# Performance work log

Hardware: AMD Instinct MI355X
Metric: run time of the kernel (lower is better)

The kernel has to match this reference:

```python
import jax, jax.numpy as jnp
import numpy as np

H = 128          # h_dim
F_IN = 3 * H     # leaf/edge feature dim
N = 65536        # number of center nodes
E = 1000000      # number of leaf nodes / edges


def setup_inputs() -> dict:
    key = jax.random.key(0)
    ks = jax.random.split(key, 8)
    center_node_attr = jax.random.normal(ks[0], (N, H), jnp.float32)
    leaf_node_all = jax.random.normal(ks[1], (E, F_IN), jnp.float32)
    node_idx = jax.random.randint(ks[2], (E,), 0, N, dtype=jnp.int32)
    gcnfeats = jax.random.normal(ks[3], (N, H), jnp.float32)
    # nn.Linear default init: U(-1/sqrt(fan_in), 1/sqrt(fan_in))
    s1 = 1.0 / np.sqrt(F_IN)
    s2 = 1.0 / np.sqrt(H)
    W1 = jax.random.uniform(ks[4], (F_IN, H), jnp.float32, -s1, s1)
    b1 = jax.random.uniform(ks[5], (H,), jnp.float32, -s1, s1)
    W2 = jax.random.uniform(ks[6], (H, H), jnp.float32, -s2, s2)
    b2 = jax.random.uniform(ks[7], (H,), jnp.float32, -s2, s2)
    return dict(center_node_attr=center_node_attr, leaf_node_all=leaf_node_all,
                node_idx=node_idx, gcnfeats=gcnfeats, W1=W1, b1=b1, W2=W2, b2=b2)


def reference(center_node_attr, leaf_node_all, node_idx, gcnfeats, W1, b1, W2, b2):
    # per-edge 2-layer MLP message: encoder(x_j)  [E, H]
    msg = jax.nn.relu(leaf_node_all @ W1 + b1) @ W2 + b2
    # scatter-max aggregation into center nodes (PyG aggr='max'); empty nodes -> 0
    neg = jnp.finfo(msg.dtype).min
    agg = jnp.full(center_node_attr.shape, neg, msg.dtype).at[node_idx].max(msg)
    agg = jnp.where(agg == neg, jnp.zeros((), msg.dtype), agg)
    lang_gcnfeats = center_node_attr + agg  # [N, H]
    # cosine similarity along dim=1 (torch eps=1e-8 clamps each norm)
    eps = 1e-8
    na = jnp.maximum(jnp.linalg.norm(gcnfeats, axis=1), eps)
    nb = jnp.maximum(jnp.linalg.norm(lang_gcnfeats, axis=1), eps)
    return jnp.sum(gcnfeats * lang_gcnfeats, axis=1) / (na * nb)  # [N]
```

## Files before the change

kernel.cpp:

```cpp
#include <hip/hip_runtime.h>

#define H_DIM 128
#define F_IN  384

typedef __bf16 v8bf __attribute__((ext_vector_type(8)));
typedef float  v4f  __attribute__((ext_vector_type(4)));

__device__ __forceinline__ unsigned enc_f32(float v) {
    unsigned u = __float_as_uint(v);
    return (u & 0x80000000u) ? ~u : (u | 0x80000000u);
}
__device__ __forceinline__ float dec_f32(unsigned e) {
    if (e == 0u) return 0.0f;
    unsigned u = (e & 0x80000000u) ? (e & 0x7fffffffu) : ~e;
    return __uint_as_float(u);
}

__global__ __launch_bounds__(256) void wconvert(const float* __restrict__ W1,
                                                const float* __restrict__ W2,
                                                __bf16* __restrict__ W1C,
                                                __bf16* __restrict__ W2T) {
    int i = blockIdx.x * 256 + threadIdx.x;
    if (i < F_IN * H_DIM) {
        int ks = i >> 12, rem = i & 4095, col = rem >> 5, kk = rem & 31;
        W1C[i] = (__bf16)W1[(ks * 32 + kk) * H_DIM + col];
    } else if (i < F_IN * H_DIM + H_DIM * H_DIM) {
        int j = i - F_IN * H_DIM;
        int col = j / H_DIM, k = j % H_DIM;
        W2T[j] = (__bf16)W2[k * H_DIM + col];
    }
}

__global__ __launch_bounds__(512) void mlp_scatter(
    const float* __restrict__ leaf, const int* __restrict__ nidx,
    const __bf16* __restrict__ W1C, const __bf16* __restrict__ W2T,
    const float* __restrict__ b1, const float* __restrict__ b2,
    unsigned* __restrict__ agg, int E)
{
    __shared__ __bf16 w1s[12][128][40];
    __shared__ int   idx_s[256];
    __shared__ float b1_s[H_DIM], b2_s[H_DIM];

    const int t  = threadIdx.x;
    const int w  = t >> 6;
    const int l  = t & 63;
    const int lr = l & 15;
    const int lg = l >> 4;
    const long e0 = (long)blockIdx.x * 256;

    if (t < 256) {
        long e = e0 + t;
        idx_s[t] = nidx[e < E ? e : (E - 1)];
    }
    if (t < H_DIM) { b1_s[t] = b1[t]; b2_s[t] = b2[t]; }

    {
        const int row = t >> 2, unit = (t & 3) * 8;
        v8bf s[12];
#pragma unroll
        for (int ks = 0; ks < 12; ++ks)
            s[ks] = *(const v8bf*)(W1C + ks * 4096 + row * 32 + unit);
#pragma unroll
        for (int ks = 0; ks < 12; ++ks)
            *(v8bf*)&w1s[ks][row][unit] = s[ks];
    }

    long erA = e0 + w * 32 + lr;
    long erB = e0 + w * 32 + 16 + lr;
    if (erA >= E) erA = E - 1;
    if (erB >= E) erB = E - 1;
    const float* arowA = leaf + erA * (long)F_IN + lg * 8;
    const float* arowB = leaf + erB * (long)F_IN + lg * 8;

    const v4f vzero = {0.f, 0.f, 0.f, 0.f};
    v4f accA[8], accB[8];
#pragma unroll
    for (int f = 0; f < 8; ++f) { accA[f] = vzero; accB[f] = vzero; }

    float4 aA0 = *(const float4*)(arowA);
    float4 aA1 = *(const float4*)(arowA + 4);
    float4 aB0 = *(const float4*)(arowB);
    float4 aB1 = *(const float4*)(arowB + 4);
    __syncthreads();

#pragma unroll
    for (int ks = 0; ks < 12; ++ks) {
        float4 nA0 = aA0, nA1 = aA1, nB0 = aB0, nB1 = aB1;
        if (ks + 1 < 12) {
            nA0 = *(const float4*)(arowA + (ks + 1) * 32);
            nA1 = *(const float4*)(arowA + (ks + 1) * 32 + 4);
            nB0 = *(const float4*)(arowB + (ks + 1) * 32);
            nB1 = *(const float4*)(arowB + (ks + 1) * 32 + 4);
        }
        v8bf afA, afB;
        afA[0] = (__bf16)aA0.x; afA[1] = (__bf16)aA0.y; afA[2] = (__bf16)aA0.z; afA[3] = (__bf16)aA0.w;
        afA[4] = (__bf16)aA1.x; afA[5] = (__bf16)aA1.y; afA[6] = (__bf16)aA1.z; afA[7] = (__bf16)aA1.w;
        afB[0] = (__bf16)aB0.x; afB[1] = (__bf16)aB0.y; afB[2] = (__bf16)aB0.z; afB[3] = (__bf16)aB0.w;
        afB[4] = (__bf16)aB1.x; afB[5] = (__bf16)aB1.y; afB[6] = (__bf16)aB1.z; afB[7] = (__bf16)aB1.w;
#pragma unroll
        for (int f = 0; f < 8; ++f) {
            v8bf bfv = *(const v8bf*)&w1s[ks][f * 16 + lr][lg * 8];
            accA[f] = __builtin_amdgcn_mfma_f32_16x16x32_bf16(afA, bfv, accA[f], 0, 0, 0);
            accB[f] = __builtin_amdgcn_mfma_f32_16x16x32_bf16(afB, bfv, accB[f], 0, 0, 0);
        }
        aA0 = nA0; aA1 = nA1; aB0 = nB0; aB1 = nB1;
    }

    __syncthreads();

    __bf16* hsp = (__bf16*)w1s;
#pragma unroll
    for (int f = 0; f < 8; ++f) {
        const float bb = b1_s[f * 16 + lr];
#pragma unroll
        for (int j = 0; j < 4; ++j) {
            float vA = fmaxf(accA[f][j] + bb, 0.0f);
            float vB = fmaxf(accB[f][j] + bb, 0.0f);
            hsp[(w * 32 + lg * 4 + j) * 136 + f * 16 + lr]        = (__bf16)vA;
            hsp[(w * 32 + 16 + lg * 4 + j) * 136 + f * 16 + lr]   = (__bf16)vB;
        }
    }

    v4f acc2A[8], acc2B[8];
#pragma unroll
    for (int f = 0; f < 8; ++f) { acc2A[f] = vzero; acc2B[f] = vzero; }
#pragma unroll
    for (int ks = 0; ks < 4; ++ks) {
        v8bf afA2 = *(const v8bf*)&hsp[(w * 32 + lr) * 136 + ks * 32 + lg * 8];
        v8bf afB2 = *(const v8bf*)&hsp[(w * 32 + 16 + lr) * 136 + ks * 32 + lg * 8];
#pragma unroll
        for (int f = 0; f < 8; ++f) {
            v8bf bfv = *(const v8bf*)(W2T + (f * 16 + lr) * H_DIM + ks * 32 + lg * 8);
            acc2A[f] = __builtin_amdgcn_mfma_f32_16x16x32_bf16(afA2, bfv, acc2A[f], 0, 0, 0);
            acc2B[f] = __builtin_amdgcn_mfma_f32_16x16x32_bf16(afB2, bfv, acc2B[f], 0, 0, 0);
        }
    }

#pragma unroll
    for (int g = 0; g < 2; ++g) {
        const int rb = w * 32 + g * 16 + lg * 4;
#pragma unroll
        for (int j = 0; j < 4; ++j) {
            const long ej = e0 + rb + j;
            if (ej < E) {
                const int node = idx_s[rb + j];
                unsigned* dst = agg + (long)node * H_DIM + lr;
#pragma unroll
                for (int f = 0; f < 8; ++f) {
                    float v = (g ? acc2B[f][j] : acc2A[f][j]) + b2_s[f * 16 + lr];
                    atomicMax(dst + f * 16, enc_f32(v));
                }
            }
        }
    }
}

__global__ __launch_bounds__(256) void cos_kernel(
    const float* __restrict__ center, const float* __restrict__ gcn,
    const unsigned* __restrict__ agg, float* __restrict__ out, int N)
{
    const int w = threadIdx.x >> 6, l = threadIdx.x & 63;
    const long row = (long)blockIdx.x * 4 + w;
    if (row >= N) return;
    const float2 g2 = *(const float2*)(gcn    + row * H_DIM + l * 2);
    const float2 c2 = *(const float2*)(center + row * H_DIM + l * 2);
    const uint2  e2 = *(const uint2*) (agg    + row * H_DIM + l * 2);
    const float l0 = c2.x + dec_f32(e2.x);
    const float l1 = c2.y + dec_f32(e2.y);
    float sgl = g2.x * l0 + g2.y * l1;
    float sgg = g2.x * g2.x + g2.y * g2.y;
    float sll = l0 * l0 + l1 * l1;
#pragma unroll
    for (int off = 32; off; off >>= 1) {
        sgl += __shfl_xor(sgl, off);
        sgg += __shfl_xor(sgg, off);
        sll += __shfl_xor(sll, off);
    }
    if (l == 0) {
        const float na = fmaxf(sqrtf(sgg), 1e-8f);
        const float nb = fmaxf(sqrtf(sll), 1e-8f);
        out[row] = sgl / (na * nb);
    }
}

extern "C" void kernel_launch(void* const* d_in, const int* in_sizes, int n_in,
                              void* d_out, int out_size, void* d_ws, size_t ws_size,
                              hipStream_t stream) {
    const float* center = (const float*)d_in[0];
    const float* leaf   = (const float*)d_in[1];
    const int*   nidx   = (const int*)  d_in[2];
    const float* gcn    = (const float*)d_in[3];
    const float* W1     = (const float*)d_in[4];
    const float* b1     = (const float*)d_in[5];
    const float* W2     = (const float*)d_in[6];
    const float* b2     = (const float*)d_in[7];

    const int E = in_sizes[2];
    const int N = in_sizes[0] / H_DIM;

    unsigned* agg = (unsigned*)d_ws;
    const size_t aggBytes = (size_t)N * H_DIM * sizeof(unsigned);
    __bf16* W1C = (__bf16*)((char*)d_ws + aggBytes);
    __bf16* W2T = W1C + (size_t)F_IN * H_DIM;

    hipMemsetAsync(agg, 0, aggBytes, stream);
    wconvert<<<(F_IN * H_DIM + H_DIM * H_DIM + 255) / 256, 256, 0, stream>>>(W1, W2, W1C, W2T);
    mlp_scatter<<<(E + 255) / 256, 512, 0, stream>>>(leaf, nidx, W1C, W2T, b1, b2, agg, E);
    cos_kernel<<<(N + 3) / 4, 256, 0, stream>>>(center, gcn, agg, (float*)d_out, N);
}
```

Before: 695.1 us.

## Double-buffer W1 k-slices in LDS and give each wave 64 edge rows

The block shrinks from 512 to 256 threads, and each wave now handles four 16-row groups instead of two. Each W1 fragment read from LDS therefore feeds four MFMAs, doubling register-level reuse. The whole-W1 LDS preload (about 120KB) becomes a double-buffered stream of 32-wide k-slices, cutting LDS to about 70KB so two blocks can co-reside. The cost is a __syncthreads per k-step and much higher VGPR pressure from 64 accumulator vectors per thread, which may cause spills or limit occupancy.

```diff
diff --git a/kernel.cpp b/kernel.cpp
--- a/kernel.cpp
+++ b/kernel.cpp
@@ -31,13 +31,15 @@
     }
 }
 
-__global__ __launch_bounds__(512) void mlp_scatter(
+__global__ __launch_bounds__(256, 2) void mlp_scatter(
     const float* __restrict__ leaf, const int* __restrict__ nidx,
     const __bf16* __restrict__ W1C, const __bf16* __restrict__ W2T,
     const float* __restrict__ b1, const float* __restrict__ b2,
     unsigned* __restrict__ agg, int E)
 {
-    __shared__ __bf16 w1s[12][128][40];
+    __shared__ char smem[69632] __attribute__((aligned(16)));
+    __bf16 (*wb)[128][40] = (__bf16 (*)[128][40])smem;
+    __bf16 (*hs)[136]     = (__bf16 (*)[136])smem;
     __shared__ int   idx_s[256];
     __shared__ float b1_s[H_DIM], b2_s[H_DIM];
 
@@ -48,97 +50,115 @@
     const int lg = l >> 4;
     const long e0 = (long)blockIdx.x * 256;
 
-    if (t < 256) {
+    {
         long e = e0 + t;
         idx_s[t] = nidx[e < E ? e : (E - 1)];
     }
     if (t < H_DIM) { b1_s[t] = b1[t]; b2_s[t] = b2[t]; }
 
+    const int colt = t >> 1, kht = (t & 1) * 16;
+
     {
-        const int row = t >> 2, unit = (t & 3) * 8;
-        v8bf s[12];
-#pragma unroll
-        for (int ks = 0; ks < 12; ++ks)
-            s[ks] = *(const v8bf*)(W1C + ks * 4096 + row * 32 + unit);
-#pragma unroll
-        for (int ks = 0; ks < 12; ++ks)
-            *(v8bf*)&w1s[ks][row][unit] = s[ks];
-    }
-
-    long erA = e0 + w * 32 + lr;
-    long erB = e0 + w * 32 + 16 + lr;
-    if (erA >= E) erA = E - 1;
-    if (erB >= E) erB = E - 1;
-    const float* arowA = leaf + erA * (long)F_IN + lg * 8;
-    const float* arowB = leaf + erB * (long)F_IN + lg * 8;
+        const v8bf* src = (const v8bf*)(W1C + colt * 32 + kht);
+        *(v8bf*)&wb[0][colt][kht]     = src[0];
+        *(v8bf*)&wb[0][colt][kht + 8] = src[1];
+    }
+
+    const float* ar[4];
+#pragma unroll
+    for (int g = 0; g < 4; ++g) {
+        long er = e0 + w * 64 + g * 16 + lr;
+        if (er >= E) er = E - 1;
+        ar[g] = leaf + er * (long)F_IN + lg * 8;
+    }
 
     const v4f vzero = {0.f, 0.f, 0.f, 0.f};
-    v4f accA[8], accB[8];
-#pragma unroll
-    for (int f = 0; f < 8; ++f) { accA[f] = vzero; accB[f] = vzero; }
-
-    float4 aA0 = *(const float4*)(arowA);
-    float4 aA1 = *(const float4*)(arowA + 4);
-    float4 aB0 = *(const float4*)(arowB);
-    float4 aB1 = *(const float4*)(arowB + 4);
+    v4f acc[4][8];
+#pragma unroll
+    for (int g = 0; g < 4; ++g)
+#pragma unroll
+        for (int f = 0; f < 8; ++f) acc[g][f] = vzero;
+
+    float4 c0[4], c1[4];
+#pragma unroll
+    for (int g = 0; g < 4; ++g) {
+        c0[g] = *(const float4*)(ar[g]);
+        c1[g] = *(const float4*)(ar[g] + 4);
+    }
     __syncthreads();
 
 #pragma unroll
     for (int ks = 0; ks < 12; ++ks) {
-        float4 nA0 = aA0, nA1 = aA1, nB0 = aB0, nB1 = aB1;
+        float4 n0[4], n1[4];
         if (ks + 1 < 12) {
-            nA0 = *(const float4*)(arowA + (ks + 1) * 32);
-            nA1 = *(const float4*)(arowA + (ks + 1) * 32 + 4);
-            nB0 = *(const float4*)(arowB + (ks + 1) * 32);
-            nB1 = *(const float4*)(arowB + (ks + 1) * 32 + 4);
-        }
-        v8bf afA, afB;
-        afA[0] = (__bf16)aA0.x; afA[1] = (__bf16)aA0.y; afA[2] = (__bf16)aA0.z; afA[3] = (__bf16)aA0.w;
-        afA[4] = (__bf16)aA1.x; afA[5] = (__bf16)aA1.y; afA[6] = (__bf16)aA1.z; afA[7] = (__bf16)aA1.w;
-        afB[0] = (__bf16)aB0.x; afB[1] = (__bf16)aB0.y; afB[2] = (__bf16)aB0.z; afB[3] = (__bf16)aB0.w;
-        afB[4] = (__bf16)aB1.x; afB[5] = (__bf16)aB1.y; afB[6] = (__bf16)aB1.z; afB[7] = (__bf16)aB1.w;
+#pragma unroll
+            for (int g = 0; g < 4; ++g) {
+                n0[g] = *(const float4*)(ar[g] + (ks + 1) * 32);
+                n1[g] = *(const float4*)(ar[g] + (ks + 1) * 32 + 4);
+            }
+            const v8bf* src = (const v8bf*)(W1C + (ks + 1) * 4096 + colt * 32 + kht);
+            const int b = (ks + 1) & 1;
+            *(v8bf*)&wb[b][colt][kht]     = src[0];
+            *(v8bf*)&wb[b][colt][kht + 8] = src[1];
+        }
+        v8bf af[4];
+#pragma unroll
+        for (int g = 0; g < 4; ++g) {
+            af[g][0] = (__bf16)c0[g].x; af[g][1] = (__bf16)c0[g].y;
+            af[g][2] = (__bf16)c0[g].z; af[g][3] = (__bf16)c0[g].w;
+            af[g][4] = (__bf16)c1[g].x; af[g][5] = (__bf16)c1[g].y;
+            af[g][6] = (__bf16)c1[g].z; af[g][7] = (__bf16)c1[g].w;
+        }
+        const int cb = ks & 1;
 #pragma unroll
         for (int f = 0; f < 8; ++f) {
-            v8bf bfv = *(const v8bf*)&w1s[ks][f * 16 + lr][lg * 8];
-            accA[f] = __builtin_amdgcn_mfma_f32_16x16x32_bf16(afA, bfv, accA[f], 0, 0, 0);
-            accB[f] = __builtin_amdgcn_mfma_f32_16x16x32_bf16(afB, bfv, accB[f], 0, 0, 0);
-        }
-        aA0 = nA0; aA1 = nA1; aB0 = nB0; aB1 = nB1;
-    }
-
-    __syncthreads();
-
-    __bf16* hsp = (__bf16*)w1s;
-#pragma unroll
-    for (int f = 0; f < 8; ++f) {
-        const float bb = b1_s[f * 16 + lr];
-#pragma unroll
-        for (int j = 0; j < 4; ++j) {
-            float vA = fmaxf(accA[f][j] + bb, 0.0f);
-            float vB = fmaxf(accB[f][j] + bb, 0.0f);
-            hsp[(w * 32 + lg * 4 + j) * 136 + f * 16 + lr]        = (__bf16)vA;
-            hsp[(w * 32 + 16 + lg * 4 + j) * 136 + f * 16 + lr]   = (__bf16)vB;
-        }
-    }
-
-    v4f acc2A[8], acc2B[8];
-#pragma unroll
-    for (int f = 0; f < 8; ++f) { acc2A[f] = vzero; acc2B[f] = vzero; }
+            v8bf bfv = *(const v8bf*)&wb[cb][f * 16 + lr][lg * 8];
+#pragma unroll
+            for (int g = 0; g < 4; ++g)
+                acc[g][f] = __builtin_amdgcn_mfma_f32_16x16x32_bf16(af[g], bfv, acc[g][f], 0, 0, 0);
+        }
+        if (ks + 1 < 12) {
+#pragma unroll
+            for (int g = 0; g < 4; ++g) { c0[g] = n0[g]; c1[g] = n1[g]; }
+        }
+        __syncthreads();
+    }
+
+#pragma unroll
+    for (int g = 0; g < 4; ++g)
+#pragma unroll
+        for (int f = 0; f < 8; ++f) {
+            const float bb = b1_s[f * 16 + lr];
+#pragma unroll
+            for (int j = 0; j < 4; ++j) {
+                float v = fmaxf(acc[g][f][j] + bb, 0.0f);
+                hs[w * 64 + g * 16 + lg * 4 + j][f * 16 + lr] = (__bf16)v;
+            }
+        }
+
+    v4f acc2[4][8];
+#pragma unroll
+    for (int g = 0; g < 4; ++g)
+#pragma unroll
+        for (int f = 0; f < 8; ++f) acc2[g][f] = vzero;
 #pragma unroll
     for (int ks = 0; ks < 4; ++ks) {
-        v8bf afA2 = *(const v8bf*)&hsp[(w * 32 + lr) * 136 + ks * 32 + lg * 8];
-        v8bf afB2 = *(const v8bf*)&hsp[(w * 32 + 16 + lr) * 136 + ks * 32 + lg * 8];
+        v8bf af2[4];
+#pragma unroll
+        for (int g = 0; g < 4; ++g)
+            af2[g] = *(const v8bf*)&hs[w * 64 + g * 16 + lr][ks * 32 + lg * 8];
 #pragma unroll
         for (int f = 0; f < 8; ++f) {
             v8bf bfv = *(const v8bf*)(W2T + (f * 16 + lr) * H_DIM + ks * 32 + lg * 8);
-            acc2A[f] = __builtin_amdgcn_mfma_f32_16x16x32_bf16(afA2, bfv, acc2A[f], 0, 0, 0);
-            acc2B[f] = __builtin_amdgcn_mfma_f32_16x16x32_bf16(afB2, bfv, acc2B[f], 0, 0, 0);
-        }
-    }
-
-#pragma unroll
-    for (int g = 0; g < 2; ++g) {
-        const int rb = w * 32 + g * 16 + lg * 4;
+#pragma unroll
+            for (int g = 0; g < 4; ++g)
+                acc2[g][f] = __builtin_amdgcn_mfma_f32_16x16x32_bf16(af2[g], bfv, acc2[g][f], 0, 0, 0);
+        }
+    }
+
+#pragma unroll
+    for (int g = 0; g < 4; ++g) {
+        const int rb = w * 64 + g * 16 + lg * 4;
 #pragma unroll
         for (int j = 0; j < 4; ++j) {
             const long ej = e0 + rb + j;
@@ -147,7 +167,7 @@
                 unsigned* dst = agg + (long)node * H_DIM + lr;
 #pragma unroll
                 for (int f = 0; f < 8; ++f) {
-                    float v = (g ? acc2B[f][j] : acc2A[f][j]) + b2_s[f * 16 + lr];
+                    float v = acc2[g][f][j] + b2_s[f * 16 + lr];
                     atomicMax(dst + f * 16, enc_f32(v));
                 }
             }
@@ -205,6 +225,6 @@
 
     hipMemsetAsync(agg, 0, aggBytes, stream);
     wconvert<<<(F_IN * H_DIM + H_DIM * H_DIM + 255) / 256, 256, 0, stream>>>(W1, W2, W1C, W2T);
-    mlp_scatter<<<(E + 255) / 256, 512, 0, stream>>>(leaf, nidx, W1C, W2T, b1, b2, agg, E);
+    mlp_scatter<<<(E + 255) / 256, 256, 0, stream>>>(leaf, nidx, W1C, W2T, b1, b2, agg, E);
     cos_kernel<<<(N + 3) / 4, 256, 0, stream>>>(center, gcn, agg, (float*)d_out, N);
 }
```

Result: faster. 626.1 us (-9.9%).
